# Kernel tuning notes

Hardware: AMD Instinct MI355X
Metric: run time of the kernel (lower is better)

Reference implementation:

```python
import jax, jax.numpy as jnp
import numpy as np

N_NODES = 100000
N_EDGES = 1600000
D_IN = 128
D_HID = 128


def _sage_conv(x, src, dst, n_nodes, W_l, b_l, W_r):
    # mean-aggregate source-node features onto destination nodes
    msg = x[src]  # [E, d] gather
    agg = jax.ops.segment_sum(msg, dst, num_segments=n_nodes)  # [N, d]
    deg = jax.ops.segment_sum(jnp.ones((src.shape[0],), x.dtype), dst,
                              num_segments=n_nodes)  # [N]
    agg = agg / jnp.maximum(deg, 1.0)[:, None]
    # lin_l(agg) + lin_r(x)  (lin_r has no bias, as in PyG SAGEConv)
    return agg @ W_l + b_l + x @ W_r


def setup_inputs() -> dict:
    key = jax.random.key(0)
    ks = jax.random.split(key, 8)
    x = jax.random.normal(ks[0], (N_NODES, D_IN), dtype=jnp.float32)
    edge_index = jax.random.randint(ks[1], (2, N_EDGES), 0, N_NODES, dtype=jnp.int32)
    s_in = 1.0 / np.sqrt(D_IN)
    s_hid = 1.0 / np.sqrt(D_HID)
    return {
        "x": x,
        "edge_index": edge_index,
        "W1_l": jax.random.normal(ks[2], (D_IN, D_HID), jnp.float32) * s_in,
        "b1_l": jnp.zeros((D_HID,), jnp.float32),
        "W1_r": jax.random.normal(ks[3], (D_IN, D_HID), jnp.float32) * s_in,
        "W2_l": jax.random.normal(ks[4], (D_HID, D_HID), jnp.float32) * s_hid,
        "b2_l": jnp.zeros((D_HID,), jnp.float32),
        "W2_r": jax.random.normal(ks[5], (D_HID, D_HID), jnp.float32) * s_hid,
    }


def reference(x, edge_index, W1_l, b1_l, W1_r, W2_l, b2_l, W2_r):
    src, dst = edge_index[0], edge_index[1]
    h = _sage_conv(x, src, dst, x.shape[0], W1_l, b1_l, W1_r)
    h = jax.nn.relu(h)
    # dropout inactive in eval mode
    h = _sage_conv(h, src, dst, x.shape[0], W2_l, b2_l, W2_r)
    return h
```

## Files before the change

### kernel.cpp

```cpp
#include <hip/hip_runtime.h>
#include <hip/hip_bf16.h>
#include <stdint.h>

typedef short short8 __attribute__((ext_vector_type(8)));
typedef float floatx4 __attribute__((ext_vector_type(4)));
typedef int intx4 __attribute__((ext_vector_type(4)));

#define NSEG 8
#define BLK_PER_SEG 256
#define SLOT 64

static __device__ __forceinline__ unsigned short f2bf(float f) {
    union { float f; unsigned u; } v; v.f = f;
    unsigned r = v.u + 0x7FFF + ((v.u >> 16) & 1);
    return (unsigned short)(r >> 16);
}
static __device__ __forceinline__ float bflo(unsigned u) {
    union { unsigned u; float f; } v; v.u = u << 16; return v.f;
}
static __device__ __forceinline__ float bfhi(unsigned u) {
    union { unsigned u; float f; } v; v.u = u & 0xFFFF0000u; return v.f;
}

__global__ void k_conv_x(const float4* __restrict__ x, ushort4* __restrict__ o, int n4) {
    int t = blockIdx.x * blockDim.x + threadIdx.x;
    if (t >= n4) return;
    float4 v = x[t];
    ushort4 r = { f2bf(v.x), f2bf(v.y), f2bf(v.z), f2bf(v.w) };
    o[t] = r;
}

__global__ void k_trans_w(const float* __restrict__ W1l, const float* __restrict__ W1r,
                          const float* __restrict__ W2l, const float* __restrict__ W2r,
                          ushort* __restrict__ wt1, ushort* __restrict__ wt2) {
    int t = blockIdx.x * blockDim.x + threadIdx.x;
    int m = t >> 15, r = t & 32767;
    int k = r >> 7, n = r & 127;
    const float* Wl = m ? W2l : W1l;
    const float* Wr = m ? W2r : W1r;
    float v = (k < 128) ? Wl[k * 128 + n] : Wr[(k - 128) * 128 + n];
    ushort* wt = m ? wt2 : wt1;
    wt[n * 256 + k] = f2bf(v);
}

static __device__ __forceinline__ int seg_of(int d, float inv_nps) {
    int s = (int)((float)d * inv_nps);
    return s > (NSEG - 1) ? (NSEG - 1) : s;
}

__global__ void __launch_bounds__(256)
k_build(const int* __restrict__ src, const int* __restrict__ dst,
        int* __restrict__ cnt, int* __restrict__ slots, int E, float inv_nps) {
    int seg  = blockIdx.x & 7;
    int bseg = blockIdx.x >> 3;
    int e4tot = E >> 2;
    int ec4 = (e4tot + BLK_PER_SEG - 1) / BLK_PER_SEG;
    int start4 = bseg * ec4, end4 = min(e4tot, start4 + ec4);
    const intx4* d4 = (const intx4*)dst;
    const intx4* s4 = (const intx4*)src;
    for (int i = start4 + (int)threadIdx.x; i < end4; i += 256) {
        intx4 dv = __builtin_nontemporal_load(&d4[i]);
        intx4 sv = __builtin_nontemporal_load(&s4[i]);
        if (seg_of(dv.x, inv_nps) == seg) { int p = atomicAdd(&cnt[dv.x], 1); slots[(size_t)dv.x * SLOT + p] = sv.x; }
        if (seg_of(dv.y, inv_nps) == seg) { int p = atomicAdd(&cnt[dv.y], 1); slots[(size_t)dv.y * SLOT + p] = sv.y; }
        if (seg_of(dv.z, inv_nps) == seg) { int p = atomicAdd(&cnt[dv.z], 1); slots[(size_t)dv.z * SLOT + p] = sv.z; }
        if (seg_of(dv.w, inv_nps) == seg) { int p = atomicAdd(&cnt[dv.w], 1); slots[(size_t)dv.w * SLOT + p] = sv.w; }
    }
    if (bseg == BLK_PER_SEG - 1 && (int)threadIdx.x < (E & 3)) {
        int e = (e4tot << 2) + threadIdx.x;
        int d = dst[e];
        if (seg_of(d, inv_nps) == seg) { int p = atomicAdd(&cnt[d], 1); slots[(size_t)d * SLOT + p] = src[e]; }
    }
}

__global__ void __launch_bounds__(256)
k_agg(const ushort* __restrict__ h, const int* __restrict__ cnt,
      const int* __restrict__ slots, ushort* __restrict__ agg, int n) {
    int node = (blockIdx.x * 256 + threadIdx.x) >> 6;
    int lane = threadIdx.x & 63;
    if (node >= n) return;
    int eg = lane >> 4;
    int c8 = lane & 15;
    int deg = cnt[node];
    const int* sl = slots + (size_t)node * SLOT;
    float a[8];
    #pragma unroll
    for (int i = 0; i < 8; ++i) a[i] = 0.f;
    for (int j = 0; j < deg; j += 8) {
        int e0 = j + eg, e1 = j + 4 + eg;
        if (e0 < deg) {
            int s = sl[e0];
            uint4 u = *(const uint4*)(h + (size_t)s * 128 + c8 * 8);
            a[0] += bflo(u.x); a[1] += bfhi(u.x);
            a[2] += bflo(u.y); a[3] += bfhi(u.y);
            a[4] += bflo(u.z); a[5] += bfhi(u.z);
            a[6] += bflo(u.w); a[7] += bfhi(u.w);
        }
        if (e1 < deg) {
            int s = sl[e1];
            uint4 u = *(const uint4*)(h + (size_t)s * 128 + c8 * 8);
            a[0] += bflo(u.x); a[1] += bfhi(u.x);
            a[2] += bflo(u.y); a[3] += bfhi(u.y);
            a[4] += bflo(u.z); a[5] += bfhi(u.z);
            a[6] += bflo(u.w); a[7] += bfhi(u.w);
        }
    }
    #pragma unroll
    for (int m = 16; m < 64; m <<= 1) {
        #pragma unroll
        for (int i = 0; i < 8; ++i) a[i] += __shfl_xor(a[i], m);
    }
    if (eg == 0) {
        float inv = 1.0f / fmaxf((float)deg, 1.0f);
        uint4 o;
        o.x = (unsigned)f2bf(a[0] * inv) | ((unsigned)f2bf(a[1] * inv) << 16);
        o.y = (unsigned)f2bf(a[2] * inv) | ((unsigned)f2bf(a[3] * inv) << 16);
        o.z = (unsigned)f2bf(a[4] * inv) | ((unsigned)f2bf(a[5] * inv) << 16);
        o.w = (unsigned)f2bf(a[6] * inv) | ((unsigned)f2bf(a[7] * inv) << 16);
        *(uint4*)(agg + (size_t)node * 128 + c8 * 8) = o;
    }
}

__global__ void __launch_bounds__(256)
k_gemm(const ushort* __restrict__ A1, const ushort* __restrict__ A2,
       const ushort* __restrict__ wt, const float* __restrict__ bias,
       int M, int mode, ushort* __restrict__ out16, float* __restrict__ out32) {
    __shared__ ushort W[128 * 264];
    int tid = threadIdx.x;
    #pragma unroll
    for (int i = 0; i < 16; ++i) {
        int t = tid + i * 256;
        int nrow = t >> 5, k8 = t & 31;
        *(uint4*)&W[nrow * 264 + k8 * 8] = *(const uint4*)&wt[nrow * 256 + k8 * 8];
    }
    __syncthreads();
    int wave = tid >> 6, lane = tid & 63;
    int l15 = lane & 15, lg = lane >> 4;
    int row_base = blockIdx.x * 64 + wave * 16;
    int r = row_base + l15;
    int rc = min(r, M - 1);
    const ushort* a1 = A1 + (size_t)rc * 128;
    const ushort* a2 = A2 + (size_t)rc * 128;
    int kg = lg * 8;
    floatx4 acc[8];
    #pragma unroll
    for (int c = 0; c < 8; ++c) acc[c] = (floatx4){0.f, 0.f, 0.f, 0.f};
    #pragma unroll
    for (int ks = 0; ks < 8; ++ks) {
        int k0 = ks * 32 + kg;
        const ushort* ap = (ks < 4) ? (a1 + k0) : (a2 + (k0 - 128));
        short8 a = *(const short8*)ap;
        #pragma unroll
        for (int c = 0; c < 8; ++c) {
            short8 b = *(const short8*)&W[(c * 16 + l15) * 264 + k0];
            acc[c] = __builtin_amdgcn_mfma_f32_16x16x32_bf16(a, b, acc[c], 0, 0, 0);
        }
    }
    #pragma unroll
    for (int c = 0; c < 8; ++c) {
        int coln = c * 16 + l15;
        float bv = bias[coln];
        #pragma unroll
        for (int i = 0; i < 4; ++i) {
            int row = row_base + lg * 4 + i;
            if (row < M) {
                float v = acc[c][i] + bv;
                if (mode == 0) {
                    v = fmaxf(v, 0.f);
                    out16[(size_t)row * 128 + coln] = f2bf(v);
                } else {
                    out32[(size_t)row * 128 + coln] = v;
                }
            }
        }
    }
}

extern "C" void kernel_launch(void* const* d_in, const int* in_sizes, int n_in,
                              void* d_out, int out_size, void* d_ws, size_t ws_size,
                              hipStream_t stream) {
    const float* x   = (const float*)d_in[0];
    const int*   ei  = (const int*)d_in[1];
    const float* W1l = (const float*)d_in[2];
    const float* b1  = (const float*)d_in[3];
    const float* W1r = (const float*)d_in[4];
    const float* W2l = (const float*)d_in[5];
    const float* b2  = (const float*)d_in[6];
    const float* W2r = (const float*)d_in[7];
    const int N = in_sizes[0] / 128;
    const int E = in_sizes[1] / 2;
    const int* srcv = ei;
    const int* dstv = ei + E;

    char* ws = (char*)d_ws;
    size_t o = 0;
    auto alloc = [&](size_t bytes) {
        o = (o + 255) & ~(size_t)255;
        char* p = ws + o; o += bytes; return p;
    };
    int*    cnt  = (int*)alloc((size_t)N * 4);
    ushort* x16  = (ushort*)alloc((size_t)N * 128 * 2);
    ushort* h16  = (ushort*)alloc((size_t)N * 128 * 2);
    ushort* agg  = (ushort*)alloc((size_t)N * 128 * 2);
    ushort* wt1  = (ushort*)alloc(128 * 256 * 2);
    ushort* wt2  = (ushort*)alloc(128 * 256 * 2);
    int* slots = (int*)d_out;

    hipMemsetAsync(cnt, 0, (size_t)N * 4, stream);

    int nps = (N + NSEG - 1) / NSEG;
    float inv_nps = 1.0f / (float)nps;

    int n4 = N * 32;
    k_conv_x<<<(n4 + 255) / 256, 256, 0, stream>>>((const float4*)x, (ushort4*)x16, n4);
    k_trans_w<<<256, 256, 0, stream>>>(W1l, W1r, W2l, W2r, wt1, wt2);

    k_build<<<NSEG * BLK_PER_SEG, 256, 0, stream>>>(srcv, dstv, cnt, slots, E, inv_nps);

    k_agg<<<(N + 3) / 4, 256, 0, stream>>>(x16, cnt, slots, agg, N);
    k_gemm<<<(N + 63) / 64, 256, 0, stream>>>(agg, x16, wt1, b1, N, 0, h16, nullptr);
    k_agg<<<(N + 3) / 4, 256, 0, stream>>>(h16, cnt, slots, agg, N);
    k_gemm<<<(N + 63) / 64, 256, 0, stream>>>(agg, h16, wt2, b2, N, 1, nullptr, (float*)d_out);
}
```

Baseline: 399.9 us.

## Partition edges by destination segment once before building slot lists

Replaces the build kernel, where every segment's blocks rescanned the whole edge list, with a two-pass scheme. The first pass buckets (src,dst) pairs into per-segment queues using a shared-memory histogram and one global atomic per segment per block. The second pass fills the per-node slot lists from each compacted queue. This removes the repeated reads of the full edge list, at the cost of an extra write and read of a partition buffer placed in the output memory. It also assumes each segment receives at most CAP edges.

```diff
diff --git a/kernel.cpp b/kernel.cpp
--- a/kernel.cpp
+++ b/kernel.cpp
@@ -5,10 +5,12 @@
 typedef short short8 __attribute__((ext_vector_type(8)));
 typedef float floatx4 __attribute__((ext_vector_type(4)));
 typedef int intx4 __attribute__((ext_vector_type(4)));
+typedef int intx2 __attribute__((ext_vector_type(2)));
 
 #define NSEG 8
-#define BLK_PER_SEG 256
 #define SLOT 64
+#define CAP 210000
+#define BLD 128
 
 static __device__ __forceinline__ unsigned short f2bf(float f) {
     union { float f; unsigned u; } v; v.f = f;
@@ -49,27 +51,55 @@
 }
 
 __global__ void __launch_bounds__(256)
-k_build(const int* __restrict__ src, const int* __restrict__ dst,
-        int* __restrict__ cnt, int* __restrict__ slots, int E, float inv_nps) {
+k_part(const int* __restrict__ src, const int* __restrict__ dst,
+       intx2* __restrict__ part, int* __restrict__ qn, int E, float inv_nps) {
+    __shared__ int hist[NSEG], base[NSEG], cur[NSEG];
+    int tid = threadIdx.x;
+    if (tid < NSEG) hist[tid] = 0;
+    __syncthreads();
+    int i4 = blockIdx.x * 256 + tid;
+    int e0 = i4 * 4;
+    intx4 dv = {0,0,0,0}, sv = {0,0,0,0};
+    int b[4] = {-1,-1,-1,-1};
+    if (e0 + 3 < E) {
+        dv = __builtin_nontemporal_load(&((const intx4*)dst)[i4]);
+        sv = __builtin_nontemporal_load(&((const intx4*)src)[i4]);
+        #pragma unroll
+        for (int c = 0; c < 4; ++c) { b[c] = seg_of(dv[c], inv_nps); atomicAdd(&hist[b[c]], 1); }
+    } else if (e0 < E) {
+        #pragma unroll
+        for (int c = 0; c < 4; ++c) {
+            if (e0 + c < E) {
+                dv[c] = dst[e0 + c]; sv[c] = src[e0 + c];
+                b[c] = seg_of(dv[c], inv_nps); atomicAdd(&hist[b[c]], 1);
+            }
+        }
+    }
+    __syncthreads();
+    if (tid < NSEG) base[tid] = atomicAdd(&qn[tid * 16], hist[tid]);
+    __syncthreads();
+    if (tid < NSEG) cur[tid] = base[tid];
+    __syncthreads();
+    #pragma unroll
+    for (int c = 0; c < 4; ++c) {
+        if (b[c] >= 0) {
+            int p = atomicAdd(&cur[b[c]], 1);
+            part[(size_t)b[c] * CAP + p] = (intx2){ sv[c], dv[c] };
+        }
+    }
+}
+
+__global__ void __launch_bounds__(256)
+k_build2(const intx2* __restrict__ part, const int* __restrict__ qn,
+         int* __restrict__ cnt, int* __restrict__ slots) {
     int seg  = blockIdx.x & 7;
     int bseg = blockIdx.x >> 3;
-    int e4tot = E >> 2;
-    int ec4 = (e4tot + BLK_PER_SEG - 1) / BLK_PER_SEG;
-    int start4 = bseg * ec4, end4 = min(e4tot, start4 + ec4);
-    const intx4* d4 = (const intx4*)dst;
-    const intx4* s4 = (const intx4*)src;
-    for (int i = start4 + (int)threadIdx.x; i < end4; i += 256) {
-        intx4 dv = __builtin_nontemporal_load(&d4[i]);
-        intx4 sv = __builtin_nontemporal_load(&s4[i]);
-        if (seg_of(dv.x, inv_nps) == seg) { int p = atomicAdd(&cnt[dv.x], 1); slots[(size_t)dv.x * SLOT + p] = sv.x; }
-        if (seg_of(dv.y, inv_nps) == seg) { int p = atomicAdd(&cnt[dv.y], 1); slots[(size_t)dv.y * SLOT + p] = sv.y; }
-        if (seg_of(dv.z, inv_nps) == seg) { int p = atomicAdd(&cnt[dv.z], 1); slots[(size_t)dv.z * SLOT + p] = sv.z; }
-        if (seg_of(dv.w, inv_nps) == seg) { int p = atomicAdd(&cnt[dv.w], 1); slots[(size_t)dv.w * SLOT + p] = sv.w; }
-    }
-    if (bseg == BLK_PER_SEG - 1 && (int)threadIdx.x < (E & 3)) {
-        int e = (e4tot << 2) + threadIdx.x;
-        int d = dst[e];
-        if (seg_of(d, inv_nps) == seg) { int p = atomicAdd(&cnt[d], 1); slots[(size_t)d * SLOT + p] = src[e]; }
+    int n = qn[seg * 16];
+    const intx2* p = part + (size_t)seg * CAP;
+    for (int i = bseg * 256 + (int)threadIdx.x; i < n; i += BLD * 256) {
+        intx2 e = __builtin_nontemporal_load(&p[i]);
+        int pos = atomicAdd(&cnt[e.y], 1);
+        slots[(size_t)e.y * SLOT + pos] = e.x;
     }
 }
 
@@ -199,14 +229,16 @@
         char* p = ws + o; o += bytes; return p;
     };
     int*    cnt  = (int*)alloc((size_t)N * 4);
+    int*    qn   = (int*)alloc(NSEG * 16 * 4);
     ushort* x16  = (ushort*)alloc((size_t)N * 128 * 2);
     ushort* h16  = (ushort*)alloc((size_t)N * 128 * 2);
     ushort* agg  = (ushort*)alloc((size_t)N * 128 * 2);
     ushort* wt1  = (ushort*)alloc(128 * 256 * 2);
     ushort* wt2  = (ushort*)alloc(128 * 256 * 2);
-    int* slots = (int*)d_out;
-
-    hipMemsetAsync(cnt, 0, (size_t)N * 4, stream);
+    int*   slots = (int*)d_out;
+    intx2* part  = (intx2*)((char*)d_out + (size_t)N * SLOT * 4);
+
+    hipMemsetAsync(cnt, 0, (size_t)((char*)qn - (char*)cnt) + NSEG * 16 * 4, stream);
 
     int nps = (N + NSEG - 1) / NSEG;
     float inv_nps = 1.0f / (float)nps;
@@ -215,7 +247,9 @@
     k_conv_x<<<(n4 + 255) / 256, 256, 0, stream>>>((const float4*)x, (ushort4*)x16, n4);
     k_trans_w<<<256, 256, 0, stream>>>(W1l, W1r, W2l, W2r, wt1, wt2);
 
-    k_build<<<NSEG * BLK_PER_SEG, 256, 0, stream>>>(srcv, dstv, cnt, slots, E, inv_nps);
+    int e4 = (E + 3) / 4;
+    k_part<<<(e4 + 255) / 256, 256, 0, stream>>>(srcv, dstv, part, qn, E, inv_nps);
+    k_build2<<<NSEG * BLD, 256, 0, stream>>>(part, qn, cnt, slots);
 
     k_agg<<<(N + 3) / 4, 256, 0, stream>>>(x16, cnt, slots, agg, N);
     k_gemm<<<(N + 63) / 64, 256, 0, stream>>>(agg, x16, wt1, b1, N, 0, h16, nullptr);
```

New measurement: 422.4 us. 5.6% more time.
